# Kernel optimization log

Hardware: AMD Instinct MI355X
Metric: run time of the kernel (lower is better)

The kernel has to match this reference:

```python
import jax, jax.numpy as jnp
import numpy as np
import math

B = 1024          # graphs per batch
N = 16384         # nodes per graph (equal-size graphs)
E = 4_000_000     # edges (unused by the output path; TopKPooling scores are edge-free)
K1 = math.ceil(0.01 * N)   # 164, pool1 ratio=0.01
K2 = math.ceil(0.1 * K1)   # 17,  pool2 ratio=0.1
K3 = math.ceil(0.1 * K2)   # 2,   pool3 ratio=0.1


def setup_inputs() -> dict:
    key = jax.random.key(0)
    ks = jax.random.split(key, 9)
    x = jax.random.normal(ks[0], (B * N, 5), dtype=jnp.float32)
    edge_index = jax.random.randint(ks[1], (2, E), 0, B * N, dtype=jnp.int64)
    batch = jnp.repeat(jnp.arange(B, dtype=jnp.int64), N)
    # TopKPooling score weights (PyG: self.weight, shape [in_channels])
    w_pool1 = jax.random.normal(ks[2], (5,), dtype=jnp.float32)
    w_pool2 = jax.random.normal(ks[3], (64,), dtype=jnp.float32)
    w_pool3 = jax.random.normal(ks[4], (64,), dtype=jnp.float32)
    # Linear layers (torch layout: W [out, in], b [out])
    W1 = jax.random.normal(ks[5], (64, 5), dtype=jnp.float32) * (1.0 / np.sqrt(5.0))
    b1 = jax.random.normal(ks[6], (64,), dtype=jnp.float32) * 0.01
    W2 = jax.random.normal(ks[7], (3, 64), dtype=jnp.float32) * (1.0 / np.sqrt(64.0))
    b2 = jax.random.normal(ks[8], (3,), dtype=jnp.float32) * 0.01
    return dict(x=x, edge_index=edge_index, batch=batch,
                w_pool1=w_pool1, W1=W1, b1=b1,
                w_pool2=w_pool2, w_pool3=w_pool3, W2=W2, b2=b2)


def _topk_pool(x, w, n_per_graph, k):
    """PyG TopKPooling on equal-size graphs.
    score = tanh((x . w) / ||w||); keep per-graph top-k nodes; x_out = x[perm] * score[perm].
    x: [B * n_per_graph, F] -> [B * k, F]
    """
    s = jnp.tanh((x @ w) / jnp.linalg.norm(w))          # [B*n] (tanh is monotonic -> same top-k)
    s = s.reshape(B, n_per_graph)                        # [B, n]
    vals, idx = jax.lax.top_k(s, k)                      # [B, k]
    xg = x.reshape(B, n_per_graph, x.shape[-1])          # [B, n, F]
    x_sel = jnp.take_along_axis(xg, idx[..., None], axis=1)  # [B, k, F]
    out = x_sel * vals[..., None]                        # gate by tanh score
    return out.reshape(B * k, x.shape[-1])


def reference(x, edge_index, batch, w_pool1, W1, b1, w_pool2, w_pool3, W2, b2):
    # edge_index/batch: TopKPooling filters edges, but the returned x never depends on
    # edge_index; batch is the equal-size segment layout encoded by (B, N) reshapes.
    h = _topk_pool(x, w_pool1, N, K1)        # pool1: [B*164, 5]
    h = h @ W1.T + b1                        # nn1:   [B*164, 64]
    h = _topk_pool(h, w_pool2, K1, K2)       # pool2: [B*17, 64]
    h = _topk_pool(h, w_pool3, K2, K3)       # pool3: [B*2, 64]
    return h @ W2.T + b2                     # nn2:   [B*2, 3]
```

## Files before the change

### kernel.cpp

```cpp
#include <hip/hip_runtime.h>
#include <math.h>

#define BGRAPH 1024
#define NNODE  16384
#define KP1    164
#define KP2    17
#define KP3    2
#define TPB    256

typedef unsigned int uint;

__device__ __forceinline__ uint sortable(float s) {
    uint u = __float_as_uint(s);
    return (u & 0x80000000u) ? ~u : (u | 0x80000000u);
}
__device__ __forceinline__ float unsortable(uint k) {
    uint u = (k & 0x80000000u) ? (k & 0x7FFFFFFFu) : ~k;
    return __uint_as_float(u);
}

__device__ __forceinline__ void bitonic256(uint* k, uint* i) {
    const int t = threadIdx.x;
    for (int sz = 2; sz <= 256; sz <<= 1) {
        for (int st = sz >> 1; st > 0; st >>= 1) {
            __syncthreads();
            int p = t ^ st;
            if (p > t) {
                uint ka = k[t], kb = k[p];
                uint ia = i[t], ib = i[p];
                bool before = (ka > kb) || (ka == kb && ia < ib);
                bool up = ((t & sz) == 0);
                if (up ? !before : before) {
                    k[t] = kb; k[p] = ka;
                    i[t] = ib; i[p] = ia;
                }
            }
        }
    }
    __syncthreads();
}

extern "C" __global__ __launch_bounds__(TPB, 3)
void net_topk_fused(const float* __restrict__ x,
                    const float* __restrict__ wp1,
                    const float* __restrict__ W1,
                    const float* __restrict__ b1,
                    const float* __restrict__ wp2,
                    const float* __restrict__ wp3,
                    const float* __restrict__ W2,
                    const float* __restrict__ b2,
                    float* __restrict__ out)
{
    __shared__ uint  hist[256];
    __shared__ uint  ckey[256];
    __shared__ uint  cidx[256];
    __shared__ float xsel[KP1 * 5];
    __shared__ float h1[KP1 * 65];
    __shared__ float s2v[KP2];
    __shared__ uint  s2row[KP2];
    __shared__ float s3v[KP3];
    __shared__ uint  s3pos[KP3];
    __shared__ uint  sh_b, sh_hi, sh_nc;

    const int tid = threadIdx.x;
    const int g   = blockIdx.x;

    const float w0 = wp1[0], w1 = wp1[1], w2 = wp1[2], w3 = wp1[3], w4 = wp1[4];
    float nq = w0 * w0;
    nq = fmaf(w1, w1, nq); nq = fmaf(w2, w2, nq);
    nq = fmaf(w3, w3, nq); nq = fmaf(w4, w4, nq);
    const float nrm1 = sqrtf(nq);

    uint key[64];
    const float4* xb = reinterpret_cast<const float4*>(x + (size_t)g * NNODE * 5);
    #pragma unroll
    for (int it = 0; it < 16; ++it) {
        const int G = tid + it * 256;
        const float4* p = xb + (size_t)G * 5;
        float4 A = p[0], B = p[1], C = p[2], D = p[3], E = p[4];
        float z;
        z = A.x * w0; z = fmaf(A.y, w1, z); z = fmaf(A.z, w2, z); z = fmaf(A.w, w3, z); z = fmaf(B.x, w4, z);
        key[it * 4 + 0] = sortable(tanhf(z / nrm1));
        z = B.y * w0; z = fmaf(B.z, w1, z); z = fmaf(B.w, w2, z); z = fmaf(C.x, w3, z); z = fmaf(C.y, w4, z);
        key[it * 4 + 1] = sortable(tanhf(z / nrm1));
        z = C.z * w0; z = fmaf(C.w, w1, z); z = fmaf(D.x, w2, z); z = fmaf(D.y, w3, z); z = fmaf(D.z, w4, z);
        key[it * 4 + 2] = sortable(tanhf(z / nrm1));
        z = D.w * w0; z = fmaf(E.x, w1, z); z = fmaf(E.y, w2, z); z = fmaf(E.z, w3, z); z = fmaf(E.w, w4, z);
        key[it * 4 + 3] = sortable(tanhf(z / nrm1));
    }

    uint Krem = KP1;
    uint prefix = 0;
    #pragma unroll
    for (int pass = 0; pass < 4; ++pass) {
        const int pshift = 32 - 8 * pass;
        const int bshift = 24 - 8 * pass;
        __syncthreads();
        hist[tid] = 0;
        __syncthreads();
        #pragma unroll
        for (int j = 0; j < 64; ++j) {
            uint k = key[j];
            bool match = (pass == 0) || ((k >> (pshift & 31)) == prefix);
            if (match) atomicAdd(&hist[(k >> bshift) & 255u], 1u);
        }
        __syncthreads();
        for (int off = 1; off < 256; off <<= 1) {
            uint v = hist[tid];
            uint w = (tid + off < 256) ? hist[tid + off] : 0u;
            __syncthreads();
            hist[tid] = v + w;
            __syncthreads();
        }
        uint Sb  = hist[tid];
        uint Sb1 = (tid < 255) ? hist[tid + 1] : 0u;
        if (Sb >= Krem && Sb1 < Krem) { sh_b = (uint)tid; sh_hi = Sb1; }
        __syncthreads();
        prefix = (prefix << 8) | sh_b;
        Krem  -= sh_hi;
    }

    if (tid == 0) sh_nc = 0;
    __syncthreads();
    #pragma unroll
    for (int j = 0; j < 64; ++j) {
        uint k = key[j];
        if (k >= prefix) {
            uint pos = atomicAdd(&sh_nc, 1u);
            if (pos < 256u) {
                ckey[pos] = k;
                cidx[pos] = 4u * (uint)tid + (uint)((j >> 2) * 1024) + (uint)(j & 3);
            }
        }
    }
    __syncthreads();
    uint nc = sh_nc; if (nc > 256u) nc = 256u;
    if ((uint)tid >= nc) { ckey[tid] = 0u; cidx[tid] = 0x7FFFFFFFu; }
    bitonic256(ckey, cidx);

    if (tid < KP1) {
        float s = unsortable(ckey[tid]);
        const float* xr = x + ((size_t)g * NNODE + cidx[tid]) * 5;
        #pragma unroll
        for (int f = 0; f < 5; ++f) xsel[tid * 5 + f] = xr[f] * s;
    }
    __syncthreads();

    for (int t = tid; t < KP1 * 64; t += TPB) {
        int i = t >> 6, c = t & 63;
        float acc = b1[c];
        #pragma unroll
        for (int f = 0; f < 5; ++f) acc = fmaf(xsel[i * 5 + f], W1[c * 5 + f], acc);
        h1[i * 65 + c] = acc;
    }
    __syncthreads();

    {
        if (tid < KP1) {
            float nw = 0.f, acc = 0.f;
            for (int f = 0; f < 64; ++f) nw = fmaf(wp2[f], wp2[f], nw);
            for (int f = 0; f < 64; ++f) acc = fmaf(h1[tid * 65 + f], wp2[f], acc);
            float s = tanhf(acc / sqrtf(nw));
            ckey[tid] = sortable(s); cidx[tid] = (uint)tid;
        } else {
            ckey[tid] = 0u; cidx[tid] = 0x7FFFFFFFu;
        }
    }
    bitonic256(ckey, cidx);
    if (tid < KP2) { s2v[tid] = unsortable(ckey[tid]); s2row[tid] = cidx[tid]; }
    __syncthreads();

    {
        if (tid < KP2) {
            float s2 = s2v[tid];
            uint row = s2row[tid];
            float nw = 0.f, acc = 0.f;
            for (int f = 0; f < 64; ++f) nw = fmaf(wp3[f], wp3[f], nw);
            for (int f = 0; f < 64; ++f) acc = fmaf(h1[row * 65 + f] * s2, wp3[f], acc);
            float s = tanhf(acc / sqrtf(nw));
            ckey[tid] = sortable(s); cidx[tid] = (uint)tid;
        } else {
            ckey[tid] = 0u; cidx[tid] = 0x7FFFFFFFu;
        }
    }
    bitonic256(ckey, cidx);
    if (tid < KP3) { s3v[tid] = unsortable(ckey[tid]); s3pos[tid] = cidx[tid]; }
    __syncthreads();

    if (tid < KP3 * 3) {
        int r = tid / 3, o = tid % 3;
        uint p2  = s3pos[r];
        uint row = s2row[p2];
        float s2 = s2v[p2], s3 = s3v[r];
        float acc = b2[o];
        for (int f = 0; f < 64; ++f) {
            float hf = (h1[row * 65 + f] * s2) * s3;
            acc = fmaf(hf, W2[o * 64 + f], acc);
        }
        out[((size_t)g * KP3 + r) * 3 + o] = acc;
    }
}

extern "C" void kernel_launch(void* const* d_in, const int* in_sizes, int n_in,
                              void* d_out, int out_size, void* d_ws, size_t ws_size,
                              hipStream_t stream) {
    const float* x   = (const float*)d_in[0];
    const float* wp1 = (const float*)d_in[3];
    const float* W1  = (const float*)d_in[4];
    const float* b1  = (const float*)d_in[5];
    const float* wp2 = (const float*)d_in[6];
    const float* wp3 = (const float*)d_in[7];
    const float* W2  = (const float*)d_in[8];
    const float* b2  = (const float*)d_in[9];
    float* out = (float*)d_out;

    hipLaunchKernelGGL(net_topk_fused, dim3(BGRAPH), dim3(TPB), 0, stream,
                       x, wp1, W1, b1, wp2, wp3, W2, b2, out);
}
```

Before: 568.5 us.

## Defer tanh to candidates, select top-256 raw scores, shrink shared memory for occupancy

Radix selection now runs on raw dot products, which preserves order because tanh is monotonic. It selects 256 candidates, and tanh is applied only to those candidates before the bitonic sort. This removes 16384 tanhf calls per graph. The full 164x64 h1 shared buffer is dropped: the pool2 scores are computed on the fly from register-held x rows, and only the 17 selected rows are materialised. The smaller shared footprint allows launch bounds of 4 blocks per SM. A risk is that more than 256 raw scores can tie at the threshold after tanh rounding, and work is duplicated when W1 is recomputed per thread.

```diff
diff --git a/kernel.cpp b/kernel.cpp
--- a/kernel.cpp
+++ b/kernel.cpp
@@ -6,6 +6,7 @@
 #define KP1    164
 #define KP2    17
 #define KP3    2
+#define KSEL   256
 #define TPB    256
 
 typedef unsigned int uint;
@@ -40,7 +41,7 @@
     __syncthreads();
 }
 
-extern "C" __global__ __launch_bounds__(TPB, 3)
+extern "C" __global__ __launch_bounds__(TPB, 4)
 void net_topk_fused(const float* __restrict__ x,
                     const float* __restrict__ wp1,
                     const float* __restrict__ W1,
@@ -55,7 +56,7 @@
     __shared__ uint  ckey[256];
     __shared__ uint  cidx[256];
     __shared__ float xsel[KP1 * 5];
-    __shared__ float h1[KP1 * 65];
+    __shared__ float h17[KP2 * 65];
     __shared__ float s2v[KP2];
     __shared__ uint  s2row[KP2];
     __shared__ float s3v[KP3];
@@ -80,16 +81,16 @@
         float4 A = p[0], B = p[1], C = p[2], D = p[3], E = p[4];
         float z;
         z = A.x * w0; z = fmaf(A.y, w1, z); z = fmaf(A.z, w2, z); z = fmaf(A.w, w3, z); z = fmaf(B.x, w4, z);
-        key[it * 4 + 0] = sortable(tanhf(z / nrm1));
+        key[it * 4 + 0] = sortable(z);
         z = B.y * w0; z = fmaf(B.z, w1, z); z = fmaf(B.w, w2, z); z = fmaf(C.x, w3, z); z = fmaf(C.y, w4, z);
-        key[it * 4 + 1] = sortable(tanhf(z / nrm1));
+        key[it * 4 + 1] = sortable(z);
         z = C.z * w0; z = fmaf(C.w, w1, z); z = fmaf(D.x, w2, z); z = fmaf(D.y, w3, z); z = fmaf(D.z, w4, z);
-        key[it * 4 + 2] = sortable(tanhf(z / nrm1));
+        key[it * 4 + 2] = sortable(z);
         z = D.w * w0; z = fmaf(E.x, w1, z); z = fmaf(E.y, w2, z); z = fmaf(E.z, w3, z); z = fmaf(E.w, w4, z);
-        key[it * 4 + 3] = sortable(tanhf(z / nrm1));
-    }
-
-    uint Krem = KP1;
+        key[it * 4 + 3] = sortable(z);
+    }
+
+    uint Krem = KSEL;
     uint prefix = 0;
     #pragma unroll
     for (int pass = 0; pass < 4; ++pass) {
@@ -134,32 +135,40 @@
         }
     }
     __syncthreads();
-    uint nc = sh_nc; if (nc > 256u) nc = 256u;
-    if ((uint)tid >= nc) { ckey[tid] = 0u; cidx[tid] = 0x7FFFFFFFu; }
+
+    {
+        uint nc = sh_nc; if (nc > 256u) nc = 256u;
+        if ((uint)tid < nc) {
+            float z = unsortable(ckey[tid]);
+            ckey[tid] = sortable(tanhf(z / nrm1));
+        } else { ckey[tid] = 0u; cidx[tid] = 0x7FFFFFFFu; }
+    }
     bitonic256(ckey, cidx);
 
+    float xr0 = 0.f, xr1 = 0.f, xr2 = 0.f, xr3 = 0.f, xr4 = 0.f;
     if (tid < KP1) {
         float s = unsortable(ckey[tid]);
         const float* xr = x + ((size_t)g * NNODE + cidx[tid]) * 5;
-        #pragma unroll
-        for (int f = 0; f < 5; ++f) xsel[tid * 5 + f] = xr[f] * s;
-    }
-    __syncthreads();
-
-    for (int t = tid; t < KP1 * 64; t += TPB) {
-        int i = t >> 6, c = t & 63;
-        float acc = b1[c];
-        #pragma unroll
-        for (int f = 0; f < 5; ++f) acc = fmaf(xsel[i * 5 + f], W1[c * 5 + f], acc);
-        h1[i * 65 + c] = acc;
+        xr0 = xr[0] * s; xr1 = xr[1] * s; xr2 = xr[2] * s; xr3 = xr[3] * s; xr4 = xr[4] * s;
+        xsel[tid * 5 + 0] = xr0; xsel[tid * 5 + 1] = xr1; xsel[tid * 5 + 2] = xr2;
+        xsel[tid * 5 + 3] = xr3; xsel[tid * 5 + 4] = xr4;
     }
     __syncthreads();
 
     {
+        float nw = 0.f;
+        for (int f = 0; f < 64; ++f) nw = fmaf(wp2[f], wp2[f], nw);
         if (tid < KP1) {
-            float nw = 0.f, acc = 0.f;
-            for (int f = 0; f < 64; ++f) nw = fmaf(wp2[f], wp2[f], nw);
-            for (int f = 0; f < 64; ++f) acc = fmaf(h1[tid * 65 + f], wp2[f], acc);
+            float acc = 0.f;
+            for (int c = 0; c < 64; ++c) {
+                float h = b1[c];
+                h = fmaf(xr0, W1[c * 5 + 0], h);
+                h = fmaf(xr1, W1[c * 5 + 1], h);
+                h = fmaf(xr2, W1[c * 5 + 2], h);
+                h = fmaf(xr3, W1[c * 5 + 3], h);
+                h = fmaf(xr4, W1[c * 5 + 4], h);
+                acc = fmaf(h, wp2[c], acc);
+            }
             float s = tanhf(acc / sqrtf(nw));
             ckey[tid] = sortable(s); cidx[tid] = (uint)tid;
         } else {
@@ -170,13 +179,23 @@
     if (tid < KP2) { s2v[tid] = unsortable(ckey[tid]); s2row[tid] = cidx[tid]; }
     __syncthreads();
 
+    for (int t = tid; t < KP2 * 64; t += TPB) {
+        int j = t >> 6, c = t & 63;
+        int row = (int)s2row[j];
+        float h = b1[c];
+        #pragma unroll
+        for (int f = 0; f < 5; ++f) h = fmaf(xsel[row * 5 + f], W1[c * 5 + f], h);
+        h17[j * 65 + c] = h;
+    }
+    __syncthreads();
+
     {
+        float nw = 0.f;
+        for (int f = 0; f < 64; ++f) nw = fmaf(wp3[f], wp3[f], nw);
         if (tid < KP2) {
             float s2 = s2v[tid];
-            uint row = s2row[tid];
-            float nw = 0.f, acc = 0.f;
-            for (int f = 0; f < 64; ++f) nw = fmaf(wp3[f], wp3[f], nw);
-            for (int f = 0; f < 64; ++f) acc = fmaf(h1[row * 65 + f] * s2, wp3[f], acc);
+            float acc = 0.f;
+            for (int c = 0; c < 64; ++c) acc = fmaf(h17[tid * 65 + c] * s2, wp3[c], acc);
             float s = tanhf(acc / sqrtf(nw));
             ckey[tid] = sortable(s); cidx[tid] = (uint)tid;
         } else {
@@ -189,13 +208,12 @@
 
     if (tid < KP3 * 3) {
         int r = tid / 3, o = tid % 3;
-        uint p2  = s3pos[r];
-        uint row = s2row[p2];
+        uint p2 = s3pos[r];
         float s2 = s2v[p2], s3 = s3v[r];
         float acc = b2[o];
-        for (int f = 0; f < 64; ++f) {
-            float hf = (h1[row * 65 + f] * s2) * s3;
-            acc = fmaf(hf, W2[o * 64 + f], acc);
+        for (int c = 0; c < 64; ++c) {
+            float hf = (h17[p2 * 65 + c] * s2) * s3;
+            acc = fmaf(hf, W2[o * 64 + c], acc);
         }
         out[((size_t)g * KP3 + r) * 3 + o] = acc;
     }
```

Measured after the change: 549.8 us. 3.3% less time.
